# Optimization experiments

Measured on AMD Instinct MI355X. Metric: run time of the kernel, lower is better.

Reference implementation:

```python
import jax, jax.numpy as jnp
import numpy as np

LN_EPS = 1e-7

def gelu(x):
    # BERT erf-based gelu
    return 0.5 * x * (1.0 + jax.lax.erf(x / jnp.sqrt(2.0).astype(x.dtype)))

def setup_inputs() -> dict:
    key = jax.random.key(0)
    k1, k2 = jax.random.split(key)
    B, S, H, I = 4, 4096, 1024, 4096
    hidden_states = jax.random.normal(k1, (B, S, H), dtype=jnp.float32)
    W = jax.random.normal(k2, (H, I), dtype=jnp.float32) * (1.0 / np.sqrt(H))
    b = jnp.zeros((I,), dtype=jnp.float32)
    ln_gamma = jnp.ones((H,), dtype=jnp.float32)
    ln_beta = jnp.zeros((H,), dtype=jnp.float32)
    return {"hidden_states": hidden_states, "ln_gamma": ln_gamma, "ln_beta": ln_beta, "W": W, "b": b}

def reference(hidden_states, ln_gamma, ln_beta, W, b):
    # LayerNorm over last dim
    mu = jnp.mean(hidden_states, axis=-1, keepdims=True)
    xc = hidden_states - mu
    var = jnp.mean(xc * xc, axis=-1, keepdims=True)
    x_norm = xc * jax.lax.rsqrt(var + LN_EPS) * ln_gamma + ln_beta
    # Linear projection [B,S,H] @ [H,I] + b, then gelu
    y = jnp.einsum('bsh,hi->bsi', x_norm, W) + b
    return gelu(y)
```

## Files before the change

### kernel.cpp

```cpp
#include <hip/hip_runtime.h>
#include <hip/hip_bf16.h>

typedef __attribute__((ext_vector_type(8))) short bf16x8;
typedef __attribute__((ext_vector_type(4))) float f32x4;

static __device__ __forceinline__ unsigned short f2bf(float f) {
    unsigned u = __builtin_bit_cast(unsigned, f);
    unsigned rounding = 0x7fffu + ((u >> 16) & 1u);
    u += rounding;
    return (unsigned short)(u >> 16);
}

static __device__ __forceinline__ void async_copy16(const void* g, void* l) {
    __builtin_amdgcn_global_load_lds(
        (const __attribute__((address_space(1))) unsigned int*)g,
        (__attribute__((address_space(3))) unsigned int*)l,
        16, 0, 0);
}

#define BARRIER() __builtin_amdgcn_s_barrier()
#define VM0()    do { asm volatile("s_waitcnt vmcnt(0)" ::: "memory"); \
                      __builtin_amdgcn_sched_barrier(0); } while (0)

static __device__ __forceinline__ float fast_gelu(float y) {
    float u = 0.7978845608028654f * y * (1.0f + 0.044715f * y * y);
    float au = fminf(fabsf(u), 9.0f);
    float e = __expf(-2.0f * au);
    float th = (1.0f - e) * __builtin_amdgcn_rcpf(1.0f + e);
    th = (u < 0.0f) ? -th : th;
    return 0.5f * y * (1.0f + th);
}

__global__ __launch_bounds__(256) void prep_kernel(
    const float* __restrict__ x, const float* __restrict__ gamma,
    const float* __restrict__ beta, unsigned short* __restrict__ Aout,
    const float* __restrict__ W, unsigned short* __restrict__ Wt) {
    __shared__ float smem[33 * 32];
    const int b = blockIdx.x;
    const int t = threadIdx.x;

    if (b < 16384) {
        const int row = b;
        const float4 v = ((const float4*)(x + (size_t)row * 1024))[t];
        float s  = v.x + v.y + v.z + v.w;
        float ss = v.x * v.x + v.y * v.y + v.z * v.z + v.w * v.w;
        #pragma unroll
        for (int off = 32; off; off >>= 1) {
            s  += __shfl_down(s, off);
            ss += __shfl_down(ss, off);
        }
        const int wid = t >> 6, lane = t & 63;
        if (lane == 0) { smem[wid] = s; smem[wid + 4] = ss; }
        __syncthreads();
        if (t == 0) {
            float S  = smem[0] + smem[1] + smem[2] + smem[3];
            float SS = smem[4] + smem[5] + smem[6] + smem[7];
            float mu = S * (1.0f / 1024.0f);
            float var = SS * (1.0f / 1024.0f) - mu * mu;
            smem[0] = mu;
            smem[1] = rsqrtf(var + 1e-7f);
        }
        __syncthreads();
        const float mu = smem[0], rs = smem[1];
        const float4 g = ((const float4*)gamma)[t];
        const float4 be = ((const float4*)beta)[t];
        ushort4 pk;
        pk.x = f2bf((v.x - mu) * rs * g.x + be.x);
        pk.y = f2bf((v.y - mu) * rs * g.y + be.y);
        pk.z = f2bf((v.z - mu) * rs * g.z + be.z);
        pk.w = f2bf((v.w - mu) * rs * g.w + be.w);
        ((ushort4*)(Aout + (size_t)row * 1024))[t] = pk;
    } else {
        const int r = b - 16384;
        const int bx = r & 127;
        const int by = r >> 7;
        float (*tile)[33] = (float(*)[33])smem;
        const int tx = t & 31;
        const int ty = t >> 5;
        #pragma unroll
        for (int i = 0; i < 4; ++i) {
            int k = by * 32 + ty + i * 8;
            tile[ty + i * 8][tx] = W[(size_t)k * 4096 + bx * 32 + tx];
        }
        __syncthreads();
        #pragma unroll
        for (int i = 0; i < 4; ++i) {
            int n = bx * 32 + ty + i * 8;
            Wt[(size_t)n * 1024 + by * 32 + tx] = f2bf(tile[tx][ty + i * 8]);
        }
    }
}

__global__ __launch_bounds__(512, 1) void gemm_kernel(
    const unsigned short* __restrict__ A, const unsigned short* __restrict__ Wt,
    const float* __restrict__ bias, float* __restrict__ out) {
    __shared__ char lds_mem[131072];

    const int bid = blockIdx.x;
    const int t = threadIdx.x;
    const int lane = t & 63;
    const int wid = t >> 6;
    const int wm = wid >> 2;
    const int wn = wid & 3;
    const int lrow = lane & 15;
    const int lk = lane >> 4;

    const int srr = t >> 3;
    const int sch = t & 7;
    const int sgc = sch ^ (srr & 7);
    const int lst = srr * 128 + sch * 16;

    const int ck0 = ((lk) ^ (lrow & 7)) * 16;
    const int ck1 = ((4 + lk) ^ (lrow & 7)) * 16;
    const int aBase = (wm * 128 + lrow) * 128;
    const int bBase = 32768 + (wn * 64 + lrow) * 128;

    char* lds0 = lds_mem;
    char* lds1 = lds_mem + 65536;

    auto tileBase = [&](int tau, const unsigned short*& gA, const unsigned short*& gB,
                        int& bm, int& bn) {
        const int swz = (tau & 7) * 128 + (tau >> 3);
        bm = swz >> 4;
        bn = swz & 15;
        gA = A  + (size_t)(bm * 256 + srr) * 1024 + sgc * 8;
        gB = Wt + (size_t)(bn * 256 + srr) * 1024 + sgc * 8;
    };

    auto stage = [&](const unsigned short* gA, const unsigned short* gB,
                     int kt, char* buf) {
        #pragma unroll
        for (int i = 0; i < 4; ++i) {
            async_copy16(gA + (size_t)(i * 64) * 1024 + kt * 64, buf + i * 64 * 128 + lst);
            async_copy16(gB + (size_t)(i * 64) * 1024 + kt * 64, buf + 32768 + i * 64 * 128 + lst);
        }
    };

    const unsigned short *gA, *gB;
    int bm, bn;
    tileBase(bid, gA, gB, bm, bn);
    stage(gA, gB, 0, lds0);
    VM0();
    BARRIER();

    const int NKT = 16;
    for (int i = 0; i < 4; ++i) {
        f32x4 acc[8][4];
        #pragma unroll
        for (int a = 0; a < 8; ++a)
            #pragma unroll
            for (int j = 0; j < 4; ++j) acc[a][j] = (f32x4)0.0f;

        float bv[4];
        #pragma unroll
        for (int ni = 0; ni < 4; ++ni) bv[ni] = bias[bn * 256 + wn * 64 + ni * 16 + lrow];

        for (int kt = 0; kt < NKT; ++kt) {
            char* cbuf = (kt & 1) ? lds1 : lds0;
            char* nbuf = (kt & 1) ? lds0 : lds1;

            bf16x8 bf[4][2];
            #pragma unroll
            for (int ni = 0; ni < 4; ++ni) {
                const char* p = cbuf + bBase + ni * 16 * 128;
                bf[ni][0] = *(const bf16x8*)(p + ck0);
                bf[ni][1] = *(const bf16x8*)(p + ck1);
            }

            if (kt + 1 < NKT) stage(gA, gB, kt + 1, nbuf);

            __builtin_amdgcn_s_setprio(1);
            #pragma unroll
            for (int mi = 0; mi < 8; ++mi) {
                const char* p = cbuf + aBase + mi * 16 * 128;
                bf16x8 a0 = *(const bf16x8*)(p + ck0);
                bf16x8 a1 = *(const bf16x8*)(p + ck1);
                #pragma unroll
                for (int ni = 0; ni < 4; ++ni) {
                    acc[mi][ni] = __builtin_amdgcn_mfma_f32_16x16x32_bf16(a0, bf[ni][0], acc[mi][ni], 0, 0, 0);
                    acc[mi][ni] = __builtin_amdgcn_mfma_f32_16x16x32_bf16(a1, bf[ni][1], acc[mi][ni], 0, 0, 0);
                }
            }
            __builtin_amdgcn_s_setprio(0);

            if (kt + 1 < NKT) {
                VM0();
                BARRIER();
            }
        }

        const int row0base = bm * 256 + wm * 128;
        const int colbase  = bn * 256 + wn * 64;
        if (i + 1 < 4) {
            tileBase(bid + 256 * (i + 1), gA, gB, bm, bn);
            stage(gA, gB, 0, lds0);
        }

        #pragma unroll
        for (int mi = 0; mi < 8; ++mi) {
            const int row0 = row0base + mi * 16 + lk * 4;
            #pragma unroll
            for (int ni = 0; ni < 4; ++ni) {
                const int col = colbase + ni * 16 + lrow;
                #pragma unroll
                for (int r = 0; r < 4; ++r) {
                    float y = acc[mi][ni][r] + bv[ni];
                    out[(size_t)(row0 + r) * 4096 + col] = fast_gelu(y);
                }
            }
        }

        if (i + 1 < 4) {
            VM0();
            BARRIER();
        }
    }
}

extern "C" void kernel_launch(void* const* d_in, const int* in_sizes, int n_in,
                              void* d_out, int out_size, void* d_ws, size_t ws_size,
                              hipStream_t stream) {
    const float* hidden = (const float*)d_in[0];
    const float* gamma  = (const float*)d_in[1];
    const float* beta   = (const float*)d_in[2];
    const float* W      = (const float*)d_in[3];
    const float* bias   = (const float*)d_in[4];
    float* out = (float*)d_out;

    unsigned short* Abf = (unsigned short*)d_ws;
    unsigned short* Wt  = (unsigned short*)((char*)d_ws + (size_t)16384 * 1024 * 2);

    prep_kernel<<<16384 + 4096, 256, 0, stream>>>(hidden, gamma, beta, Abf, W, Wt);
    gemm_kernel<<<256, 512, 0, stream>>>(Abf, Wt, bias, out);
}
```

Before: 182.8 us.

## Split K-step into two half-phases with staggered A/B async loads

Each K-step of the GEMM is split into two halves: the first loads B fragments and half of the A fragments, issues the next B tile prefetch and does half the MFMAs; the second loads the remaining A fragments, issues the next A prefetch and finishes the MFMAs. Partial vmcnt waits replace full drains so loads stay in flight across barriers. The next output tile's first K-slice is prefetched during the last K-step, so the epilogue no longer ends in a full drain and barrier. The cost is an extra barrier per K-step and more intricate wait-count bookkeeping, which could stall or be fragile.

```diff
diff --git a/kernel.cpp b/kernel.cpp
--- a/kernel.cpp
+++ b/kernel.cpp
@@ -19,8 +19,9 @@
 }
 
 #define BARRIER() __builtin_amdgcn_s_barrier()
-#define VM0()    do { asm volatile("s_waitcnt vmcnt(0)" ::: "memory"); \
+#define VMCNT(N) do { asm volatile("s_waitcnt vmcnt(" #N ")" ::: "memory"); \
                       __builtin_amdgcn_sched_barrier(0); } while (0)
+#define VM0() VMCNT(0)
 
 static __device__ __forceinline__ float fast_gelu(float y) {
     float u = 0.7978845608028654f * y * (1.0f + 0.044715f * y * y);
@@ -118,8 +119,9 @@
     char* lds0 = lds_mem;
     char* lds1 = lds_mem + 65536;
 
-    auto tileBase = [&](int tau, const unsigned short*& gA, const unsigned short*& gB,
-                        int& bm, int& bn) {
+    const unsigned short *gA, *gB;
+    int bm, bn;
+    auto tileBase = [&](int tau) {
         const int swz = (tau & 7) * 128 + (tau >> 3);
         bm = swz >> 4;
         bn = swz & 15;
@@ -127,37 +129,44 @@
         gB = Wt + (size_t)(bn * 256 + srr) * 1024 + sgc * 8;
     };
 
-    auto stage = [&](const unsigned short* gA, const unsigned short* gB,
-                     int kt, char* buf) {
-        #pragma unroll
-        for (int i = 0; i < 4; ++i) {
-            async_copy16(gA + (size_t)(i * 64) * 1024 + kt * 64, buf + i * 64 * 128 + lst);
-            async_copy16(gB + (size_t)(i * 64) * 1024 + kt * 64, buf + 32768 + i * 64 * 128 + lst);
-        }
+    auto stageB = [&](const unsigned short* pB, int kt, char* buf) {
+        #pragma unroll
+        for (int i = 0; i < 4; ++i)
+            async_copy16(pB + (size_t)(i * 64) * 1024 + kt * 64,
+                         buf + 32768 + i * 8192 + lst);
     };
-
-    const unsigned short *gA, *gB;
-    int bm, bn;
-    tileBase(bid, gA, gB, bm, bn);
-    stage(gA, gB, 0, lds0);
+    auto stageA = [&](const unsigned short* pA, int kt, char* buf) {
+        async_copy16(pA + kt * 64,                      buf + lst);
+        async_copy16(pA + (size_t)131072 + kt * 64,     buf + 16384 + lst);
+        async_copy16(pA + (size_t)65536  + kt * 64,     buf + 8192  + lst);
+        async_copy16(pA + (size_t)196608 + kt * 64,     buf + 24576 + lst);
+    };
+
+    tileBase(bid);
+    stageB(gB, 0, lds0);
+    stageA(gA, 0, lds0);
     VM0();
     BARRIER();
 
     const int NKT = 16;
     for (int i = 0; i < 4; ++i) {
+        const int bmc = bm, bnc = bn;
+        float bv[4];
+        #pragma unroll
+        for (int ni = 0; ni < 4; ++ni) bv[ni] = bias[bnc * 256 + wn * 64 + ni * 16 + lrow];
+
         f32x4 acc[8][4];
         #pragma unroll
         for (int a = 0; a < 8; ++a)
             #pragma unroll
             for (int j = 0; j < 4; ++j) acc[a][j] = (f32x4)0.0f;
-
-        float bv[4];
-        #pragma unroll
-        for (int ni = 0; ni < 4; ++ni) bv[ni] = bias[bn * 256 + wn * 64 + ni * 16 + lrow];
 
         for (int kt = 0; kt < NKT; ++kt) {
             char* cbuf = (kt & 1) ? lds1 : lds0;
             char* nbuf = (kt & 1) ? lds0 : lds1;
+            const bool haveNext = (kt < NKT - 1) || (i < 3);
+            if (kt == NKT - 1 && i < 3) tileBase(bid + 256 * (i + 1));
+            const int ktn = (kt < NKT - 1) ? kt + 1 : 0;
 
             bf16x8 bf[4][2];
             #pragma unroll
@@ -166,53 +175,67 @@
                 bf[ni][0] = *(const bf16x8*)(p + ck0);
                 bf[ni][1] = *(const bf16x8*)(p + ck1);
             }
-
-            if (kt + 1 < NKT) stage(gA, gB, kt + 1, nbuf);
-
+            bf16x8 af[4][2];
+            #pragma unroll
+            for (int mi = 0; mi < 4; ++mi) {
+                const char* p = cbuf + aBase + mi * 16 * 128;
+                af[mi][0] = *(const bf16x8*)(p + ck0);
+                af[mi][1] = *(const bf16x8*)(p + ck1);
+            }
+            if (haveNext) stageB(gB, ktn, nbuf);
             __builtin_amdgcn_s_setprio(1);
             #pragma unroll
-            for (int mi = 0; mi < 8; ++mi) {
-                const char* p = cbuf + aBase + mi * 16 * 128;
-                bf16x8 a0 = *(const bf16x8*)(p + ck0);
-                bf16x8 a1 = *(const bf16x8*)(p + ck1);
+            for (int mi = 0; mi < 4; ++mi)
                 #pragma unroll
                 for (int ni = 0; ni < 4; ++ni) {
-                    acc[mi][ni] = __builtin_amdgcn_mfma_f32_16x16x32_bf16(a0, bf[ni][0], acc[mi][ni], 0, 0, 0);
-                    acc[mi][ni] = __builtin_amdgcn_mfma_f32_16x16x32_bf16(a1, bf[ni][1], acc[mi][ni], 0, 0, 0);
+                    acc[mi][ni] = __builtin_amdgcn_mfma_f32_16x16x32_bf16(af[mi][0], bf[ni][0], acc[mi][ni], 0, 0, 0);
+                    acc[mi][ni] = __builtin_amdgcn_mfma_f32_16x16x32_bf16(af[mi][1], bf[ni][1], acc[mi][ni], 0, 0, 0);
                 }
-            }
             __builtin_amdgcn_s_setprio(0);
-
-            if (kt + 1 < NKT) {
+            if (!haveNext) {
                 VM0();
-                BARRIER();
-            }
-        }
-
-        const int row0base = bm * 256 + wm * 128;
-        const int colbase  = bn * 256 + wn * 64;
-        if (i + 1 < 4) {
-            tileBase(bid + 256 * (i + 1), gA, gB, bm, bn);
-            stage(gA, gB, 0, lds0);
+            } else if (kt > 0) {
+                VMCNT(4);
+            }
+            BARRIER();
+
+            bf16x8 ag[4][2];
+            #pragma unroll
+            for (int mi = 0; mi < 4; ++mi) {
+                const char* p = cbuf + aBase + (64 + mi * 16) * 128;
+                ag[mi][0] = *(const bf16x8*)(p + ck0);
+                ag[mi][1] = *(const bf16x8*)(p + ck1);
+            }
+            if (haveNext) stageA(gA, ktn, nbuf);
+            __builtin_amdgcn_s_setprio(1);
+            #pragma unroll
+            for (int mi = 0; mi < 4; ++mi)
+                #pragma unroll
+                for (int ni = 0; ni < 4; ++ni) {
+                    acc[4 + mi][ni] = __builtin_amdgcn_mfma_f32_16x16x32_bf16(ag[mi][0], bf[ni][0], acc[4 + mi][ni], 0, 0, 0);
+                    acc[4 + mi][ni] = __builtin_amdgcn_mfma_f32_16x16x32_bf16(ag[mi][1], bf[ni][1], acc[4 + mi][ni], 0, 0, 0);
+                }
+            __builtin_amdgcn_s_setprio(0);
+            if (kt == NKT - 1) {
+                VM0();
+            } else {
+                VMCNT(2);
+            }
+            BARRIER();
         }
 
         #pragma unroll
         for (int mi = 0; mi < 8; ++mi) {
-            const int row0 = row0base + mi * 16 + lk * 4;
+            const int row0 = bmc * 256 + wm * 128 + mi * 16 + lk * 4;
             #pragma unroll
             for (int ni = 0; ni < 4; ++ni) {
-                const int col = colbase + ni * 16 + lrow;
+                const int col = bnc * 256 + wn * 64 + ni * 16 + lrow;
                 #pragma unroll
                 for (int r = 0; r < 4; ++r) {
                     float y = acc[mi][ni][r] + bv[ni];
                     out[(size_t)(row0 + r) * 4096 + col] = fast_gelu(y);
                 }
             }
-        }
-
-        if (i + 1 < 4) {
-            VM0();
-            BARRIER();
         }
     }
 }
```

Result: faster. 177.9 us (median of 2 runs) (-2.7%).
